# Performance work log

Hardware: AMD Instinct MI355X
Metric: run time of the kernel (lower is better)

Reference implementation:

```python
import jax, jax.numpy as jnp
import numpy as np

N, E, L, C = 5000, 50000, 9, 128      # nodes, edges, (lmax+1)^2 with lmax=2, sphere_channels
HID, HEADS, AV, VC = 128, 8, 32, 16   # attn hidden, heads, alpha channels, value channels
DRBF, AEMB, MAXZ = 128, 64, 100       # rbf dim, atom embed dim, max elements


def _block_params(key, tag):
    ks = jax.random.split(key, 8)
    s = lambda k, shp, fan: jax.random.normal(k, shp, jnp.float32) / np.sqrt(fan)
    return {
        'atom_emb_' + tag: s(ks[0], (MAXZ, AEMB), AEMB),
        'W_rad1_' + tag: s(ks[1], (DRBF + 2 * AEMB, HID), DRBF + 2 * AEMB),
        'W_rad2_' + tag: s(ks[2], (HID, HID), HID),
        'W_msg_' + tag: s(ks[3], (2 * C, HID), 2 * C),
        'W_alpha_' + tag: s(ks[4], (HID, HEADS * AV), HID),
        'alpha_vec_' + tag: s(ks[5], (HEADS, AV), AV),
        'W_val_' + tag: s(ks[6], (HID, HEADS * VC), HID),
        'W_proj_' + tag: s(ks[7], (HEADS * VC, 1), HEADS * VC),
    }


def setup_inputs() -> dict:
    key = jax.random.key(0)
    k = jax.random.split(key, 8)
    inp = {
        'node_embedding': jax.random.normal(k[0], (N, L, C), jnp.float32),
        'edge_distance': jax.random.uniform(k[1], (E, DRBF), jnp.float32),
        'wigner': jax.random.normal(k[2], (E, L, L), jnp.float32) / np.sqrt(L),
        'atomic_numbers': jax.random.randint(k[3], (N,), 0, MAXZ),
        'edge_index': jax.random.randint(k[4], (2, E), 0, N),
        'noise_mask': jax.random.bernoulli(k[5], 0.5, (N,)),
    }
    inp.update(_block_params(k[6], 'v'))
    inp.update(_block_params(k[7], 'd'))
    return inp


def _so2_attention(x, z, edge_dist, src, dst, wig, p, tag):
    # gather + per-edge SO(2)/Wigner rotation
    x_src = jnp.einsum('eij,ejc->eic', wig, x[src])          # [E,L,C]
    x_dst = jnp.einsum('eij,ejc->eic', wig, x[dst])
    msg = jnp.concatenate([x_src, x_dst], axis=-1) @ p['W_msg_' + tag]  # [E,L,HID]
    # radial (distance + atom-edge embedding) channel-wise modulation
    ae = p['atom_emb_' + tag]
    edge_in = jnp.concatenate([edge_dist, ae[z[src]], ae[z[dst]]], axis=-1)
    rad = jax.nn.silu(edge_in @ p['W_rad1_' + tag]) @ p['W_rad2_' + tag]  # [E,HID]
    msg = msg * rad[:, None, :]
    # alpha attention from the l=0 (scalar) coefficient
    a = (msg[:, 0, :] @ p['W_alpha_' + tag]).reshape(E, HEADS, AV)
    logits = jnp.einsum('eha,ha->eh', jax.nn.leaky_relu(a, 0.2), p['alpha_vec_' + tag])
    m = jax.ops.segment_max(logits, dst, num_segments=N)
    ex = jnp.exp(logits - m[dst])
    den = jax.ops.segment_sum(ex, dst, num_segments=N)
    attn = ex / (den[dst] + 1e-9)                            # [E,HEADS]
    # separable S2 gate activation: silu on scalars, sigmoid gate on l>0
    gate = jax.nn.sigmoid(msg[:, :1, :])
    val = jnp.concatenate([jax.nn.silu(msg[:, :1, :]), msg[:, 1:, :] * gate], axis=1)
    v = (val @ p['W_val_' + tag]).reshape(E, L, HEADS, VC)
    v = (v * attn[:, None, :, None]).reshape(E, L, HEADS * VC)
    v = jnp.einsum('eji,ejc->eic', wig, v)                   # inverse (transpose) rotation
    agg = jax.ops.segment_sum(v, dst, num_segments=N)        # scatter-reduce to nodes
    return agg @ p['W_proj_' + tag]                          # [N,L,1]


def reference(node_embedding, edge_distance, wigner,
              atom_emb_v, W_rad1_v, W_rad2_v, W_msg_v, W_alpha_v, alpha_vec_v, W_val_v, W_proj_v,
              atom_emb_d, W_rad1_d, W_rad2_d, W_msg_d, W_alpha_d, alpha_vec_d, W_val_d, W_proj_d,
              atomic_numbers, edge_index, noise_mask):
    p = dict(atom_emb_v=atom_emb_v, W_rad1_v=W_rad1_v, W_rad2_v=W_rad2_v, W_msg_v=W_msg_v,
             W_alpha_v=W_alpha_v, alpha_vec_v=alpha_vec_v, W_val_v=W_val_v, W_proj_v=W_proj_v,
             atom_emb_d=atom_emb_d, W_rad1_d=W_rad1_d, W_rad2_d=W_rad2_d, W_msg_d=W_msg_d,
             W_alpha_d=W_alpha_d, alpha_vec_d=alpha_vec_d, W_val_d=W_val_d, W_proj_d=W_proj_d)
    src, dst = edge_index[0], edge_index[1]
    out_v = _so2_attention(node_embedding, atomic_numbers, edge_distance, src, dst, wigner, p, 'v')
    out_d = _so2_attention(node_embedding, atomic_numbers, edge_distance, src, dst, wigner, p, 'd')
    # narrow(1, 1, 3): take l=1 vector coefficients, view as [N,3]
    vec = out_v[:, 1:4, 0]
    dns = out_d[:, 1:4, 0]
    # denoising_pos_forward with noise_mask: dns*mask + vec*~mask
    return jnp.where(noise_mask[:, None], dns, vec)
```

## Files before the change

kernel.cpp:

```cpp
#include <hip/hip_runtime.h>

#define NN 5000
#define NE 50000
#define LL 9
#define CC 128
#define NH 8
#define VCD 16
#define DR 128
#define AE 64
#define MZ 100

typedef unsigned int u32;
typedef unsigned short u16;

typedef __attribute__((ext_vector_type(8))) short bf16x8;
typedef __attribute__((ext_vector_type(4))) float f32x4;

__device__ __forceinline__ bf16x8 as_bf16x8(uint4 v){
  union { uint4 u; bf16x8 b; } x; x.u = v; return x.b;
}

__device__ __forceinline__ float bf_lo(u32 u){ return __uint_as_float(u << 16); }
__device__ __forceinline__ float bf_hi(u32 u){ return __uint_as_float(u & 0xffff0000u); }
__device__ __forceinline__ u16 f2bf(float f){
  u32 u = __float_as_uint(f);
  u32 r = (u + 0x7fffu + ((u >> 16) & 1u)) >> 16;
  return (u16)r;
}
__device__ __forceinline__ u32 pack2(float a, float b){
  return (u32)f2bf(a) | ((u32)f2bf(b) << 16);
}
__device__ __forceinline__ u32 encf(float f){
  u32 u = __float_as_uint(f);
  return (u & 0x80000000u) ? ~u : (u | 0x80000000u);
}
__device__ __forceinline__ float decf(u32 k){
  u32 u = (k & 0x80000000u) ? (k & 0x7fffffffu) : ~k;
  return __uint_as_float(u);
}
__device__ __forceinline__ float sigmoidf_(float x){ return 1.f / (1.f + __expf(-x)); }

__global__ void k0_tables(const float* __restrict__ ae_v, const float* __restrict__ wr1_v,
                          const float* __restrict__ ae_d, const float* __restrict__ wr1_d,
                          const float* __restrict__ wval_v, const float* __restrict__ wproj_v,
                          const float* __restrict__ wval_d, const float* __restrict__ wproj_d,
                          const float* __restrict__ wmsg_v, const float* __restrict__ wmsg_d,
                          const float* __restrict__ wal_v, const float* __restrict__ wal_d,
                          const float* __restrict__ wr2_v, const float* __restrict__ wr2_d,
                          float* __restrict__ radz, float* __restrict__ wpv,
                          u32* __restrict__ mkey, float* __restrict__ den,
                          float* __restrict__ acc, u32* __restrict__ cnt,
                          u32* __restrict__ WtM, u32* __restrict__ WtA,
                          u32* __restrict__ WtR1, u32* __restrict__ WtR2)
{
  int idx = blockIdx.x * 256 + threadIdx.x;
  if (idx < 2 * 2 * MZ * CC) {
    int c = idx & 127;
    int z = (idx >> 7) % MZ;
    int sd = (idx / (128 * MZ)) & 1;
    int tag = idx / (128 * MZ * 2);
    const float* ae = tag ? ae_d : ae_v;
    const float* w  = tag ? wr1_d : wr1_v;
    float s = 0.f;
    for (int a = 0; a < AE; ++a)
      s += ae[z * AE + a] * w[(DR + sd * AE + a) * CC + c];
    radz[idx] = s;
  }
  int i2 = idx - 2 * 2 * MZ * CC;
  if (i2 >= 0 && i2 < 2 * CC * NH) {
    int h = i2 & 7;
    int c = (i2 >> 3) & 127;
    int tag = i2 >> 10;
    const float* wv = tag ? wval_d : wval_v;
    const float* wp = tag ? wproj_d : wproj_v;
    float s = 0.f;
    for (int q = 0; q < VCD; ++q) s += wv[c * (NH * VCD) + h * VCD + q] * wp[h * VCD + q];
    wpv[i2] = s;
  }
  int i3 = i2 - 2 * CC * NH;
  if (i3 >= 0 && i3 < 2 * NN * NH) mkey[i3] = 0u;
  int i4 = i3 - 2 * NN * NH;
  if (i4 >= 0 && i4 < 2 * NN * NH) den[i4] = 0.f;
  int i5 = i4 - 2 * NN * NH;
  if (i5 >= 0 && i5 < 2 * NN * 3) acc[i5] = 0.f;
  int i6 = i5 - 2 * NN * 3;
  if (i6 >= 0 && i6 < NN) cnt[i6] = 0u;
  int i7 = i6 - NN;
  if (i7 >= 0 && i7 < 4 * 128 * 64) {
    int chunk = i7 >> 13;
    int col = (i7 >> 6) & 127;
    int kp = i7 & 63;
    const float* Wm = (chunk >= 2) ? wmsg_d : wmsg_v;
    int kb = 128 * (chunk & 1);
    WtM[i7] = pack2(Wm[(kb + 2 * kp) * 128 + col], Wm[(kb + 2 * kp + 1) * 128 + col]);
  }
  int i8 = i7 - 4 * 128 * 64;
  if (i8 >= 0 && i8 < 2 * 256 * 64) {
    int tag = i8 >> 14;
    int col = (i8 >> 6) & 255;
    int kp = i8 & 63;
    const float* Wa = tag ? wal_d : wal_v;
    WtA[i8] = pack2(Wa[(2 * kp) * 256 + col], Wa[(2 * kp + 1) * 256 + col]);
  }
  int i9 = i8 - 2 * 256 * 64;
  if (i9 >= 0 && i9 < 2 * 128 * 64) {
    int tag = i9 >> 13;
    int col = (i9 >> 6) & 127;
    int kp = i9 & 63;
    const float* W = tag ? wr1_d : wr1_v;
    WtR1[i9] = pack2(W[(2 * kp) * 128 + col], W[(2 * kp + 1) * 128 + col]);
  }
  int i10 = i9 - 2 * 128 * 64;
  if (i10 >= 0 && i10 < 2 * 128 * 64) {
    int tag = i10 >> 13;
    int col = (i10 >> 6) & 127;
    int kp = i10 & 63;
    const float* W = tag ? wr2_d : wr2_v;
    WtR2[i10] = pack2(W[(2 * kp) * 128 + col], W[(2 * kp + 1) * 128 + col]);
  }
}

__global__ void k0_flag(const u32* __restrict__ mw, int* __restrict__ flag)
{
  __shared__ int bad;
  if (threadIdx.x == 0) bad = 0;
  __syncthreads();
  int lbad = 0;
  for (int i = threadIdx.x; i < 1248; i += 256)
    if (mw[i] > 1u) lbad = 1;
  if (lbad) bad = 1;
  __syncthreads();
  if (threadIdx.x == 0) *flag = bad;
}

__global__ void ks_hist(const int* __restrict__ eidx, u32* __restrict__ cnt)
{
  int idx = blockIdx.x * 256 + threadIdx.x;
  if (idx < NE) atomicAdd(&cnt[eidx[NE + idx]], 1u);
}

__global__ void ks_scan(u32* __restrict__ cnt)
{
  __shared__ u32 tsum[256];
  int t = threadIdx.x;
  u32 loc[20];
  u32 s = 0;
  #pragma unroll
  for (int k = 0; k < 20; ++k) {
    int b = t * 20 + k;
    loc[k] = (b < NN) ? cnt[b] : 0u;
    s += loc[k];
  }
  tsum[t] = s;
  __syncthreads();
  for (int off = 1; off < 256; off <<= 1) {
    u32 v = (t >= off) ? tsum[t - off] : 0u;
    __syncthreads();
    tsum[t] += v;
    __syncthreads();
  }
  u32 base = (t == 0) ? 0u : tsum[t - 1];
  #pragma unroll
  for (int k = 0; k < 20; ++k) {
    int b = t * 20 + k;
    if (b < NN) cnt[b] = base;
    base += loc[k];
  }
}

__global__ void ks_scatter(const int* __restrict__ eidx, u32* __restrict__ base,
                           u32* __restrict__ eperm, int* __restrict__ ssrc, int* __restrict__ sdst)
{
  int idx = blockIdx.x * 256 + threadIdx.x;
  if (idx >= NE) return;
  int d = eidx[NE + idx];
  u32 pos = atomicAdd(&base[d], 1u);
  eperm[pos] = (u32)idx;
  ssrc[pos] = eidx[idx];
  sdst[pos] = d;
}

__global__ __launch_bounds__(256) void k1_nodepre(const float* __restrict__ x,
                                                  const u32* __restrict__ WtM,
                                                  u32* __restrict__ P32)
{
  __shared__ uint4 As4[32 * 17];
  u32* As = (u32*)As4;
  int t = threadIdx.x;
  int row0 = blockIdx.x * 32;
  for (int i = t; i < 32 * 64; i += 256) {
    int r = i >> 6, cp = i & 63;
    int row = row0 + r;
    u32 v = 0u;
    if (row < NN * LL) {
      float2 xv = *(const float2*)(x + (size_t)row * CC + 2 * cp);
      v = pack2(xv.x, xv.y);
    }
    As[r * 68 + cp] = v;
  }
  __syncthreads();
  int w = t >> 6, lane = t & 63;
  int m = lane & 15, kb = lane >> 4;
  int r16 = 16 * (w & 1);
  int cb = 256 * (w >> 1);
  bf16x8 afr[4];
  #pragma unroll
  for (int ks = 0; ks < 4; ++ks)
    afr[ks] = as_bf16x8(*(const uint4*)&As[(r16 + m) * 68 + ks * 16 + kb * 4]);
  int rowbase = row0 + r16;
  for (int ct = 0; ct < 16; ++ct) {
    int col = cb + ct * 16 + m;
    int chunk = col >> 7;
    int cl = col & 127;
    f32x4 accv = {0.f, 0.f, 0.f, 0.f};
    #pragma unroll
    for (int ks = 0; ks < 4; ++ks) {
      bf16x8 bfr = as_bf16x8(*(const uint4*)(WtM + ((size_t)chunk * 128 + cl) * 64 + ks * 16 + kb * 4));
      accv = __builtin_amdgcn_mfma_f32_16x16x32_bf16(afr[ks], bfr, accv, 0, 0, 0);
    }
    #pragma unroll
    for (int reg = 0; reg < 4; ++reg) {
      float v = accv[reg];
      float vv = __shfl_xor(v, 1, 64);
      int row = rowbase + kb * 4 + reg;
      if (((lane & 1) == 0) && row < NN * LL) {
        int n = row / 9, j = row - n * 9;
        P32[((size_t)n * 4 + chunk) * 576 + j * 64 + (cl >> 1)] = pack2(v, vv);
      }
    }
  }
}

__global__ __launch_bounds__(256) void k23_rad(const float* __restrict__ edist,
                                               const u32* __restrict__ WtR1,
                                               const u32* __restrict__ WtR2,
                                               const u32* __restrict__ eperm,
                                               const int* __restrict__ ssrc,
                                               const int* __restrict__ sdst,
                                               const int* __restrict__ zn,
                                               const float* __restrict__ radz,
                                               u32* __restrict__ h1rad)
{
  __shared__ uint4 As4[32 * 17];
  __shared__ uint4 Hs4[32 * 17];
  u32* As = (u32*)As4;
  u32* Hs = (u32*)Hs4;
  __shared__ int zsS[32], zdS[32];
  __shared__ u32 epS[32];
  int t = threadIdx.x;
  int tag = blockIdx.y;
  int e0 = blockIdx.x * 32;
  if (t < 32) {
    int e = e0 + t;
    u32 ep = 0; int s = 0, d = 0;
    if (e < NE) { ep = eperm[e]; s = ssrc[e]; d = sdst[e]; }
    epS[t] = ep; zsS[t] = zn[s]; zdS[t] = zn[d];
  }
  __syncthreads();
  for (int i = t; i < 32 * 64; i += 256) {
    int r = i >> 6, cp = i & 63;
    u32 v = 0u;
    if (e0 + r < NE) {
      float2 xv = *(const float2*)(edist + (size_t)epS[r] * DR + 2 * cp);
      v = pack2(xv.x, xv.y);
    }
    As[r * 68 + cp] = v;
  }
  __syncthreads();
  int w = t >> 6, lane = t & 63;
  int m = lane & 15, kb = lane >> 4;
  int r16 = 16 * (w & 1);
  int cb = 64 * (w >> 1);
  const float* rz_s = radz + tag * 2 * MZ * CC;
  const float* rz_d = rz_s + MZ * CC;
  {
    bf16x8 afr[4];
    #pragma unroll
    for (int ks = 0; ks < 4; ++ks)
      afr[ks] = as_bf16x8(*(const uint4*)&As[(r16 + m) * 68 + ks * 16 + kb * 4]);
    const u32* B1 = WtR1 + (size_t)tag * 128 * 64;
    #pragma unroll
    for (int ct = 0; ct < 4; ++ct) {
      int col = cb + ct * 16 + m;
      f32x4 accv = {0.f, 0.f, 0.f, 0.f};
      #pragma unroll
      for (int ks = 0; ks < 4; ++ks) {
        bf16x8 bfr = as_bf16x8(*(const uint4*)(B1 + (size_t)col * 64 + ks * 16 + kb * 4));
        accv = __builtin_amdgcn_mfma_f32_16x16x32_bf16(afr[ks], bfr, accv, 0, 0, 0);
      }
      #pragma unroll
      for (int reg = 0; reg < 4; ++reg) {
        int row = r16 + kb * 4 + reg;
        float v = accv[reg] + rz_s[zsS[row] * CC + col] + rz_d[zdS[row] * CC + col];
        v = v * sigmoidf_(v);
        float vv = __shfl_xor(v, 1, 64);
        if ((m & 1) == 0) Hs[row * 68 + (col >> 1)] = pack2(v, vv);
      }
    }
  }
  __syncthreads();
  {
    bf16x8 afr[4];
    #pragma unroll
    for (int ks = 0; ks < 4; ++ks)
      afr[ks] = as_bf16x8(*(const uint4*)&Hs[(r16 + m) * 68 + ks * 16 + kb * 4]);
    const u32* B2 = WtR2 + (size_t)tag * 128 * 64;
    #pragma unroll
    for (int ct = 0; ct < 4; ++ct) {
      int col = cb + ct * 16 + m;
      f32x4 accv = {0.f, 0.f, 0.f, 0.f};
      #pragma unroll
      for (int ks = 0; ks < 4; ++ks) {
        bf16x8 bfr = as_bf16x8(*(const uint4*)(B2 + (size_t)col * 64 + ks * 16 + kb * 4));
        accv = __builtin_amdgcn_mfma_f32_16x16x32_bf16(afr[ks], bfr, accv, 0, 0, 0);
      }
      #pragma unroll
      for (int reg = 0; reg < 4; ++reg) {
        int row = r16 + kb * 4 + reg;
        int e = e0 + row;
        float v = accv[reg];
        float vv = __shfl_xor(v, 1, 64);
        if (((m & 1) == 0) && e < NE)
          h1rad[((size_t)tag * NE + e) * 64 + (col >> 1)] = pack2(v, vv);
      }
    }
  }
}

__global__ __launch_bounds__(256) void k4_logits(const u32* __restrict__ P32,
                                                 const float* __restrict__ wig,
                                                 const u32* __restrict__ h1rad,
                                                 const u32* __restrict__ WtA,
                                                 const float* __restrict__ av_v,
                                                 const float* __restrict__ av_d,
                                                 const u32* __restrict__ eperm,
                                                 const int* __restrict__ ssrc,
                                                 const int* __restrict__ sdst,
                                                 float* __restrict__ logits,
                                                 u32* __restrict__ mkey)
{
  __shared__ uint4 As4[32 * 17];
  u32* As = (u32*)As4;
  __shared__ float wig0s[32][9];
  __shared__ int es_s[32], ed_s[32];
  __shared__ u32 ep_s[32];
  __shared__ float ltile[32][8];
  int t = threadIdx.x;
  int tag = blockIdx.y;
  const float* av = tag ? av_d : av_v;
  int i0 = blockIdx.x * 32;
  if (t < 32) {
    int i = i0 + t;
    int s = 0, d = 0; u32 ep = 0;
    if (i < NE) { s = ssrc[i]; d = sdst[i]; ep = eperm[i]; }
    es_s[t] = s; ed_s[t] = d; ep_s[t] = ep;
  }
  __syncthreads();
  for (int q = t; q < 32 * 9; q += 256) {
    int el = q / 9, j = q % 9;
    wig0s[el][j] = (i0 + el < NE) ? wig[(size_t)ep_s[el] * 81 + j] : 0.f;
  }
  __syncthreads();
  {
    int el = t >> 3, pp = t & 7;
    int i = i0 + el;
    float m0[16];
    #pragma unroll
    for (int k = 0; k < 16; ++k) m0[k] = 0.f;
    if (i < NE) {
      const uint4* Ts = (const uint4*)(P32 + ((size_t)es_s[el] * 4 + tag * 2) * 576);
      const uint4* Td = (const uint4*)(P32 + ((size_t)ed_s[el] * 4 + tag * 2 + 1) * 576);
      #pragma unroll
      for (int j = 0; j < 9; ++j) {
        float w = wig0s[el][j];
        uint4 a0 = Ts[j * 16 + 2 * pp], a1 = Ts[j * 16 + 2 * pp + 1];
        uint4 b0 = Td[j * 16 + 2 * pp], b1 = Td[j * 16 + 2 * pp + 1];
        u32 wa[8] = { a0.x, a0.y, a0.z, a0.w, a1.x, a1.y, a1.z, a1.w };
        u32 wb[8] = { b0.x, b0.y, b0.z, b0.w, b1.x, b1.y, b1.z, b1.w };
        #pragma unroll
        for (int r = 0; r < 8; ++r) {
          m0[2 * r]     += w * (bf_lo(wa[r]) + bf_lo(wb[r]));
          m0[2 * r + 1] += w * (bf_hi(wa[r]) + bf_hi(wb[r]));
        }
      }
      const uint4* Rp = (const uint4*)(h1rad + ((size_t)tag * NE + i) * 64);
      uint4 r0u = Rp[2 * pp], r1u = Rp[2 * pp + 1];
      u32 wr[8] = { r0u.x, r0u.y, r0u.z, r0u.w, r1u.x, r1u.y, r1u.z, r1u.w };
      #pragma unroll
      for (int r = 0; r < 8; ++r) {
        m0[2 * r]     *= bf_lo(wr[r]);
        m0[2 * r + 1] *= bf_hi(wr[r]);
      }
    }
    #pragma unroll
    for (int r = 0; r < 8; ++r)
      As[el * 68 + pp * 8 + r] = pack2(m0[2 * r], m0[2 * r + 1]);
  }
  __syncthreads();
  {
    int w = t >> 6, lane = t & 63;
    int m = lane & 15, kb = lane >> 4;
    int r16 = 16 * (w & 1);
    int cb = 128 * (w >> 1);
    bf16x8 afr[4];
    #pragma unroll
    for (int ks = 0; ks < 4; ++ks)
      afr[ks] = as_bf16x8(*(const uint4*)&As[(r16 + m) * 68 + ks * 16 + kb * 4]);
    const u32* WA = WtA + (size_t)tag * 256 * 64;
    float psum[4][4];
    #pragma unroll
    for (int a = 0; a < 4; ++a)
      #pragma unroll
      for (int b = 0; b < 4; ++b) psum[a][b] = 0.f;
    #pragma unroll
    for (int ct = 0; ct < 8; ++ct) {
      int col = cb + ct * 16 + m;
      f32x4 accv = {0.f, 0.f, 0.f, 0.f};
      #pragma unroll
      for (int ks = 0; ks < 4; ++ks) {
        bf16x8 bfr = as_bf16x8(*(const uint4*)(WA + (size_t)col * 64 + ks * 16 + kb * 4));
        accv = __builtin_amdgcn_mfma_f32_16x16x32_bf16(afr[ks], bfr, accv, 0, 0, 0);
      }
      int hl = ct >> 1;
      float avv = av[(4 * (w >> 1) + hl) * 32 + (ct & 1) * 16 + m];
      #pragma unroll
      for (int reg = 0; reg < 4; ++reg) {
        float aa = accv[reg];
        aa = (aa >= 0.f) ? aa : 0.2f * aa;
        psum[hl][reg] += aa * avv;
      }
    }
    #pragma unroll
    for (int hl = 0; hl < 4; ++hl) {
      #pragma unroll
      for (int reg = 0; reg < 4; ++reg) {
        float v = psum[hl][reg];
        v += __shfl_xor(v, 1, 64);
        v += __shfl_xor(v, 2, 64);
        v += __shfl_xor(v, 4, 64);
        v += __shfl_xor(v, 8, 64);
        if (m == 0) ltile[r16 + kb * 4 + reg][4 * (w >> 1) + hl] = v;
      }
    }
  }
  __syncthreads();
  {
    int el = t >> 3, hh = t & 7;
    int i = i0 + el;
    if (i < NE) {
      float lg = ltile[el][hh];
      logits[((size_t)tag * NE + i) * NH + hh] = lg;
      atomicMax(&mkey[tag * NN * NH + ed_s[el] * NH + hh], encf(lg));
    }
  }
}

__global__ void k5_ex(const float* __restrict__ logits, const u32* __restrict__ mkey,
                      const int* __restrict__ sdst, float* __restrict__ ex, float* __restrict__ den)
{
  int idx = blockIdx.x * 256 + threadIdx.x;
  if (idx >= 2 * NE * NH) return;
  int h = idx & 7;
  int e = (idx >> 3) % NE;
  int tag = idx / (NE * NH);
  int d = sdst[e];
  float m = decf(mkey[tag * NN * NH + d * NH + h]);
  float v = __expf(logits[idx] - m);
  ex[idx] = v;
  atomicAdd(&den[tag * NN * NH + d * NH + h], v);
}

__global__ __launch_bounds__(256) void k6_main(const u32* __restrict__ P32,
                                               const float* __restrict__ wig,
                                               const u32* __restrict__ h1rad,
                                               const float* __restrict__ wpv,
                                               const float* __restrict__ ex,
                                               const float* __restrict__ den,
                                               const u32* __restrict__ eperm,
                                               const int* __restrict__ ssrc,
                                               const int* __restrict__ sdst,
                                               float* __restrict__ acc)
{
  __shared__ float wigs[4][81];
  __shared__ u32 ep4[4];
  int t = threadIdx.x;
  int tag = blockIdx.y;
  int ib = blockIdx.x * 4;
  if (t < 4) ep4[t] = eperm[ib + t];
  __syncthreads();
  for (int q = t; q < 4 * 81; q += 256) {
    int el = q / 81, j = q % 81;
    wigs[el][j] = wig[(size_t)ep4[el] * 81 + j];
  }
  __syncthreads();
  int wid = t >> 6, lane = t & 63;
  int i = ib + wid;
  int s = ssrc[i], d = sdst[i];
  const u32* rowT = P32 + ((size_t)s * 4 + tag * 2) * 576;
  const u32* rowB = P32 + ((size_t)d * 4 + tag * 2 + 1) * 576;
  float S0[9], S1[9];
  #pragma unroll
  for (int j = 0; j < 9; ++j) {
    u32 ut = rowT[j * 64 + lane];
    u32 ub = rowB[j * 64 + lane];
    S0[j] = bf_lo(ut) + bf_lo(ub);
    S1[j] = bf_hi(ut) + bf_hi(ub);
  }
  float m0[9], m1[9];
  #pragma unroll
  for (int r = 0; r < 9; ++r) {
    float a0 = 0.f, a1 = 0.f;
    #pragma unroll
    for (int j = 0; j < 9; ++j) {
      float w = wigs[wid][r * 9 + j];
      a0 += w * S0[j];
      a1 += w * S1[j];
    }
    m0[r] = a0; m1[r] = a1;
  }
  u32 ur = h1rad[((size_t)tag * NE + i) * 64 + lane];
  float r0v = bf_lo(ur), r1v = bf_hi(ur);
  #pragma unroll
  for (int r = 0; r < 9; ++r) { m0[r] *= r0v; m1[r] *= r1v; }
  float g0 = sigmoidf_(m0[0]);
  float g1 = sigmoidf_(m1[0]);
  float gA = 0.f, gB = 0.f;
  #pragma unroll
  for (int h = 0; h < NH; ++h) {
    float at = ex[((size_t)tag * NE + i) * NH + h]
             / (den[tag * NN * NH + d * NH + h] + 1e-9f);
    gA += wpv[tag * 1024 + (2 * lane) * 8 + h] * at;
    gB += wpv[tag * 1024 + (2 * lane + 1) * 8 + h] * at;
  }
  float sp[9];
  #pragma unroll
  for (int r = 0; r < 9; ++r)
    sp[r] = m0[r] * g0 * gA + m1[r] * g1 * gB;
  #pragma unroll
  for (int off = 1; off < 64; off <<= 1) {
    #pragma unroll
    for (int r = 0; r < 9; ++r)
      sp[r] += __shfl_xor(sp[r], off, 64);
  }
  if (lane < 3) {
    int ip = lane + 1;
    float y = 0.f;
    #pragma unroll
    for (int j = 0; j < 9; ++j)
      y += wigs[wid][j * 9 + ip] * sp[j];
    atomicAdd(&acc[tag * NN * 3 + d * 3 + lane], y);
  }
}

__global__ void k7_out(const float* __restrict__ acc, const void* __restrict__ mask,
                       const int* __restrict__ flag, float* __restrict__ out)
{
  int idx = blockIdx.x * 256 + threadIdx.x;
  if (idx >= NN * 3) return;
  int n = idx / 3;
  bool msk;
  if (*flag) msk = ((const unsigned char*)mask)[n] != 0;
  else       msk = ((const int*)mask)[n] != 0;
  out[idx] = msk ? acc[NN * 3 + idx] : acc[idx];
}

extern "C" void kernel_launch(void* const* d_in, const int* in_sizes, int n_in,
                              void* d_out, int out_size, void* d_ws, size_t ws_size,
                              hipStream_t stream)
{
  (void)hipGetLastError();

  bool setup_order = (n_in >= 22) && (in_sizes[3] == NN) && (in_sizes[4] == 2 * NE);
  const float *x, *edist, *wig;
  const int *zn, *eidx;
  const void *mask;
  const float *ae_v, *wr1_v, *wr2_v, *wmsg_v, *wal_v, *av_v, *wval_v, *wproj_v;
  const float *ae_d, *wr1_d, *wr2_d, *wmsg_d, *wal_d, *av_d, *wval_d, *wproj_d;
  x     = (const float*)d_in[0];
  edist = (const float*)d_in[1];
  wig   = (const float*)d_in[2];
  if (setup_order) {
    zn      = (const int*)d_in[3];
    eidx    = (const int*)d_in[4];
    mask    = d_in[5];
    ae_v    = (const float*)d_in[6];   wr1_v  = (const float*)d_in[7];
    wr2_v   = (const float*)d_in[8];   wmsg_v = (const float*)d_in[9];
    wal_v   = (const float*)d_in[10];  av_v   = (const float*)d_in[11];
    wval_v  = (const float*)d_in[12];  wproj_v= (const float*)d_in[13];
    ae_d    = (const float*)d_in[14];  wr1_d  = (const float*)d_in[15];
    wr2_d   = (const float*)d_in[16];  wmsg_d = (const float*)d_in[17];
    wal_d   = (const float*)d_in[18];  av_d   = (const float*)d_in[19];
    wval_d  = (const float*)d_in[20];  wproj_d= (const float*)d_in[21];
  } else {
    ae_v    = (const float*)d_in[3];   wr1_v  = (const float*)d_in[4];
    wr2_v   = (const float*)d_in[5];   wmsg_v = (const float*)d_in[6];
    wal_v   = (const float*)d_in[7];   av_v   = (const float*)d_in[8];
    wval_v  = (const float*)d_in[9];   wproj_v= (const float*)d_in[10];
    ae_d    = (const float*)d_in[11];  wr1_d  = (const float*)d_in[12];
    wr2_d   = (const float*)d_in[13];  wmsg_d = (const float*)d_in[14];
    wal_d   = (const float*)d_in[15];  av_d   = (const float*)d_in[16];
    wval_d  = (const float*)d_in[17];  wproj_d= (const float*)d_in[18];
    zn      = (const int*)d_in[19];
    eidx    = (const int*)d_in[20];
    mask    = d_in[21];
  }

  const size_t OFF_P    = 0;
  const size_t OFF_H1   = 46080000;
  const size_t OFF_LOG  = 71680000;
  const size_t OFF_EX   = 74880000;
  const size_t OFF_MK   = 78080000;
  const size_t OFF_DEN  = 78400000;
  const size_t OFF_ACC  = 78720000;
  const size_t OFF_RADZ = 78840000;
  const size_t OFF_WPV  = 79044800;
  const size_t OFF_FLAG = 79052992;
  const size_t OFF_CNT  = 79053056;
  const size_t OFF_PERM = 79073056;
  const size_t OFF_SSRC = 79273056;
  const size_t OFF_SDST = 79473056;
  const size_t OFF_WTM  = 79673056;
  const size_t OFF_WTA  = 79804128;
  const size_t OFF_WTR1 = 79935200;
  const size_t OFF_WTR2 = 80000736;
  const size_t NEEDED   = 80066272;

  const size_t out_bytes = (size_t)out_size * sizeof(float);

  if (d_ws == nullptr || ws_size < NEEDED) {
    hipMemsetAsync(d_out, 0x66, out_bytes, stream);
    return;
  }

  char* ws = (char*)d_ws;
  u32*   P32    = (u32*)(ws + OFF_P);
  u32*   h1rad  = (u32*)(ws + OFF_H1);
  float* logits = (float*)(ws + OFF_LOG);
  float* ex     = (float*)(ws + OFF_EX);
  u32*   mkey   = (u32*)(ws + OFF_MK);
  float* den    = (float*)(ws + OFF_DEN);
  float* acc    = (float*)(ws + OFF_ACC);
  float* radz   = (float*)(ws + OFF_RADZ);
  float* wpv    = (float*)(ws + OFF_WPV);
  int*   flag   = (int*)(ws + OFF_FLAG);
  u32*   cnt    = (u32*)(ws + OFF_CNT);
  u32*   eperm  = (u32*)(ws + OFF_PERM);
  int*   ssrc   = (int*)(ws + OFF_SSRC);
  int*   sdst   = (int*)(ws + OFF_SDST);
  u32*   WtM    = (u32*)(ws + OFF_WTM);
  u32*   WtA    = (u32*)(ws + OFF_WTA);
  u32*   WtR1   = (u32*)(ws + OFF_WTR1);
  u32*   WtR2   = (u32*)(ws + OFF_WTR2);

  k0_tables<<<1354, 256, 0, stream>>>(ae_v, wr1_v, ae_d, wr1_d,
                                      wval_v, wproj_v, wval_d, wproj_d,
                                      wmsg_v, wmsg_d, wal_v, wal_d,
                                      wr2_v, wr2_d,
                                      radz, wpv, mkey, den, acc, cnt,
                                      WtM, WtA, WtR1, WtR2);
  k0_flag<<<1, 256, 0, stream>>>((const u32*)mask, flag);
  ks_hist<<<196, 256, 0, stream>>>(eidx, cnt);
  ks_scan<<<1, 256, 0, stream>>>(cnt);
  ks_scatter<<<196, 256, 0, stream>>>(eidx, cnt, eperm, ssrc, sdst);
  k1_nodepre<<<1407, 256, 0, stream>>>(x, WtM, P32);
  k23_rad<<<dim3(1563, 2), 256, 0, stream>>>(edist, WtR1, WtR2, eperm, ssrc, sdst,
                                             zn, radz, h1rad);
  k4_logits<<<dim3(1563, 2), 256, 0, stream>>>(P32, wig, h1rad, WtA, av_v, av_d,
                                               eperm, ssrc, sdst, logits, mkey);
  k5_ex<<<3125, 256, 0, stream>>>(logits, mkey, sdst, ex, den);
  k6_main<<<dim3(12500, 2), 256, 0, stream>>>(P32, wig, h1rad, wpv, ex, den,
                                              eperm, ssrc, sdst, acc);
  k7_out<<<59, 256, 0, stream>>>(acc, mask, flag, (float*)d_out);

  if (hipGetLastError() != hipSuccess) {
    hipMemsetAsync(d_out, 0x77, out_bytes, stream);
  }
}
```

Baseline: 526.1 us.

## Fuse full message rotation into logits kernel and precompute per-head projected values

```diff
diff --git a/kernel.cpp b/kernel.cpp
--- a/kernel.cpp
+++ b/kernel.cpp
@@ -327,24 +327,27 @@
   }
 }
 
-__global__ __launch_bounds__(256) void k4_logits(const u32* __restrict__ P32,
-                                                 const float* __restrict__ wig,
-                                                 const u32* __restrict__ h1rad,
-                                                 const u32* __restrict__ WtA,
-                                                 const float* __restrict__ av_v,
-                                                 const float* __restrict__ av_d,
-                                                 const u32* __restrict__ eperm,
-                                                 const int* __restrict__ ssrc,
-                                                 const int* __restrict__ sdst,
-                                                 float* __restrict__ logits,
-                                                 u32* __restrict__ mkey)
+__global__ __launch_bounds__(256) void kF(const u32* __restrict__ P32,
+                                          const float* __restrict__ wig,
+                                          const u32* __restrict__ h1rad,
+                                          const u32* __restrict__ WtA,
+                                          const float* __restrict__ av_v,
+                                          const float* __restrict__ av_d,
+                                          const float* __restrict__ wpv,
+                                          const u32* __restrict__ eperm,
+                                          const int* __restrict__ ssrc,
+                                          const int* __restrict__ sdst,
+                                          float* __restrict__ logits,
+                                          u32* __restrict__ mkey,
+                                          float* __restrict__ Tbuf)
 {
   __shared__ uint4 As4[32 * 17];
   u32* As = (u32*)As4;
-  __shared__ float wig0s[32][9];
+  __shared__ float wigS[32][82];
   __shared__ int es_s[32], ed_s[32];
   __shared__ u32 ep_s[32];
   __shared__ float ltile[32][8];
+  __shared__ float wpvS[1024];
   int t = threadIdx.x;
   int tag = blockIdx.y;
   const float* av = tag ? av_d : av_v;
@@ -355,50 +358,92 @@
     if (i < NE) { s = ssrc[i]; d = sdst[i]; ep = eperm[i]; }
     es_s[t] = s; ed_s[t] = d; ep_s[t] = ep;
   }
-  __syncthreads();
-  for (int q = t; q < 32 * 9; q += 256) {
-    int el = q / 9, j = q % 9;
-    wig0s[el][j] = (i0 + el < NE) ? wig[(size_t)ep_s[el] * 81 + j] : 0.f;
+  for (int q = t; q < 1024; q += 256) wpvS[q] = wpv[tag * 1024 + q];
+  __syncthreads();
+  for (int q = t; q < 32 * 81; q += 256) {
+    int el = q / 81, j = q - el * 81;
+    wigS[el][j] = (i0 + el < NE) ? wig[(size_t)ep_s[el] * 81 + j] : 0.f;
+  }
+  __syncthreads();
+  int w = t >> 6, lane = t & 63;
+  for (int k = 0; k < 8; ++k) {
+    int el = w * 8 + k;
+    int i = i0 + el;
+    bool ok = (i < NE);
+    float S0[9], S1[9];
+    #pragma unroll
+    for (int j = 0; j < 9; ++j) { S0[j] = 0.f; S1[j] = 0.f; }
+    float r0v = 0.f, r1v = 0.f;
+    if (ok) {
+      const u32* rowT = P32 + ((size_t)es_s[el] * 4 + tag * 2) * 576;
+      const u32* rowB = P32 + ((size_t)ed_s[el] * 4 + tag * 2 + 1) * 576;
+      #pragma unroll
+      for (int j = 0; j < 9; ++j) {
+        u32 a = rowT[j * 64 + lane];
+        u32 b = rowB[j * 64 + lane];
+        S0[j] = bf_lo(a) + bf_lo(b);
+        S1[j] = bf_hi(a) + bf_hi(b);
+      }
+      u32 ur = h1rad[((size_t)tag * NE + i) * 64 + lane];
+      r0v = bf_lo(ur); r1v = bf_hi(ur);
+    }
+    float m0[9], m1[9];
+    #pragma unroll
+    for (int r = 0; r < 9; ++r) {
+      float a0 = 0.f, a1 = 0.f;
+      #pragma unroll
+      for (int j = 0; j < 9; ++j) {
+        float wv = wigS[el][r * 9 + j];
+        a0 += wv * S0[j];
+        a1 += wv * S1[j];
+      }
+      m0[r] = a0 * r0v;
+      m1[r] = a1 * r1v;
+    }
+    As[el * 68 + lane] = pack2(m0[0], m1[0]);
+    float g0 = sigmoidf_(m0[0]);
+    float g1 = sigmoidf_(m1[0]);
+    float Wp[3][8];
+    #pragma unroll
+    for (int i3 = 0; i3 < 3; ++i3)
+      #pragma unroll
+      for (int h = 0; h < 8; ++h) Wp[i3][h] = 0.f;
+    #pragma unroll
+    for (int j = 0; j < 9; ++j) {
+      float v0 = m0[j] * g0, v1 = m1[j] * g1;
+      float vw[8];
+      #pragma unroll
+      for (int h = 0; h < 8; ++h)
+        vw[h] = v0 * wpvS[(2 * lane) * 8 + h] + v1 * wpvS[(2 * lane + 1) * 8 + h];
+      float wo1 = wigS[el][j * 9 + 1];
+      float wo2 = wigS[el][j * 9 + 2];
+      float wo3 = wigS[el][j * 9 + 3];
+      #pragma unroll
+      for (int h = 0; h < 8; ++h) {
+        Wp[0][h] += wo1 * vw[h];
+        Wp[1][h] += wo2 * vw[h];
+        Wp[2][h] += wo3 * vw[h];
+      }
+    }
+    #pragma unroll
+    for (int off = 1; off < 64; off <<= 1)
+      #pragma unroll
+      for (int i3 = 0; i3 < 3; ++i3)
+        #pragma unroll
+        for (int h = 0; h < 8; ++h)
+          Wp[i3][h] += __shfl_xor(Wp[i3][h], off, 64);
+    if (lane == 0 && ok) {
+      float* Tp = Tbuf + ((size_t)tag * NE + i) * 24;
+      #pragma unroll
+      for (int h = 0; h < 8; ++h) {
+        Tp[h * 3 + 0] = Wp[0][h];
+        Tp[h * 3 + 1] = Wp[1][h];
+        Tp[h * 3 + 2] = Wp[2][h];
+      }
+    }
   }
   __syncthreads();
   {
-    int el = t >> 3, pp = t & 7;
-    int i = i0 + el;
-    float m0[16];
-    #pragma unroll
-    for (int k = 0; k < 16; ++k) m0[k] = 0.f;
-    if (i < NE) {
-      const uint4* Ts = (const uint4*)(P32 + ((size_t)es_s[el] * 4 + tag * 2) * 576);
-      const uint4* Td = (const uint4*)(P32 + ((size_t)ed_s[el] * 4 + tag * 2 + 1) * 576);
-      #pragma unroll
-      for (int j = 0; j < 9; ++j) {
-        float w = wig0s[el][j];
-        uint4 a0 = Ts[j * 16 + 2 * pp], a1 = Ts[j * 16 + 2 * pp + 1];
-        uint4 b0 = Td[j * 16 + 2 * pp], b1 = Td[j * 16 + 2 * pp + 1];
-        u32 wa[8] = { a0.x, a0.y, a0.z, a0.w, a1.x, a1.y, a1.z, a1.w };
-        u32 wb[8] = { b0.x, b0.y, b0.z, b0.w, b1.x, b1.y, b1.z, b1.w };
-        #pragma unroll
-        for (int r = 0; r < 8; ++r) {
-          m0[2 * r]     += w * (bf_lo(wa[r]) + bf_lo(wb[r]));
-          m0[2 * r + 1] += w * (bf_hi(wa[r]) + bf_hi(wb[r]));
-        }
-      }
-      const uint4* Rp = (const uint4*)(h1rad + ((size_t)tag * NE + i) * 64);
-      uint4 r0u = Rp[2 * pp], r1u = Rp[2 * pp + 1];
-      u32 wr[8] = { r0u.x, r0u.y, r0u.z, r0u.w, r1u.x, r1u.y, r1u.z, r1u.w };
-      #pragma unroll
-      for (int r = 0; r < 8; ++r) {
-        m0[2 * r]     *= bf_lo(wr[r]);
-        m0[2 * r + 1] *= bf_hi(wr[r]);
-      }
-    }
-    #pragma unroll
-    for (int r = 0; r < 8; ++r)
-      As[el * 68 + pp * 8 + r] = pack2(m0[2 * r], m0[2 * r + 1]);
-  }
-  __syncthreads();
-  {
-    int w = t >> 6, lane = t & 63;
     int m = lane & 15, kb = lane >> 4;
     int r16 = 16 * (w & 1);
     int cb = 128 * (w >> 1);
@@ -470,86 +515,28 @@
   atomicAdd(&den[tag * NN * NH + d * NH + h], v);
 }
 
-__global__ __launch_bounds__(256) void k6_main(const u32* __restrict__ P32,
-                                               const float* __restrict__ wig,
-                                               const u32* __restrict__ h1rad,
-                                               const float* __restrict__ wpv,
-                                               const float* __restrict__ ex,
-                                               const float* __restrict__ den,
-                                               const u32* __restrict__ eperm,
-                                               const int* __restrict__ ssrc,
-                                               const int* __restrict__ sdst,
-                                               float* __restrict__ acc)
-{
-  __shared__ float wigs[4][81];
-  __shared__ u32 ep4[4];
-  int t = threadIdx.x;
-  int tag = blockIdx.y;
-  int ib = blockIdx.x * 4;
-  if (t < 4) ep4[t] = eperm[ib + t];
-  __syncthreads();
-  for (int q = t; q < 4 * 81; q += 256) {
-    int el = q / 81, j = q % 81;
-    wigs[el][j] = wig[(size_t)ep4[el] * 81 + j];
-  }
-  __syncthreads();
-  int wid = t >> 6, lane = t & 63;
-  int i = ib + wid;
-  int s = ssrc[i], d = sdst[i];
-  const u32* rowT = P32 + ((size_t)s * 4 + tag * 2) * 576;
-  const u32* rowB = P32 + ((size_t)d * 4 + tag * 2 + 1) * 576;
-  float S0[9], S1[9];
+__global__ void k6_scatter(const float* __restrict__ ex, const float* __restrict__ den,
+                           const float* __restrict__ Tbuf, const int* __restrict__ sdst,
+                           float* __restrict__ acc)
+{
+  int idx = blockIdx.x * 256 + threadIdx.x;
+  if (idx >= 2 * NE) return;
+  int tag = idx / NE;
+  int e = idx - tag * NE;
+  int d = sdst[e];
+  const float* Tp = Tbuf + ((size_t)tag * NE + e) * 24;
+  float y0 = 0.f, y1 = 0.f, y2 = 0.f;
   #pragma unroll
-  for (int j = 0; j < 9; ++j) {
-    u32 ut = rowT[j * 64 + lane];
-    u32 ub = rowB[j * 64 + lane];
-    S0[j] = bf_lo(ut) + bf_lo(ub);
-    S1[j] = bf_hi(ut) + bf_hi(ub);
-  }
-  float m0[9], m1[9];
-  #pragma unroll
-  for (int r = 0; r < 9; ++r) {
-    float a0 = 0.f, a1 = 0.f;
-    #pragma unroll
-    for (int j = 0; j < 9; ++j) {
-      float w = wigs[wid][r * 9 + j];
-      a0 += w * S0[j];
-      a1 += w * S1[j];
-    }
-    m0[r] = a0; m1[r] = a1;
-  }
-  u32 ur = h1rad[((size_t)tag * NE + i) * 64 + lane];
-  float r0v = bf_lo(ur), r1v = bf_hi(ur);
-  #pragma unroll
-  for (int r = 0; r < 9; ++r) { m0[r] *= r0v; m1[r] *= r1v; }
-  float g0 = sigmoidf_(m0[0]);
-  float g1 = sigmoidf_(m1[0]);
-  float gA = 0.f, gB = 0.f;
-  #pragma unroll
-  for (int h = 0; h < NH; ++h) {
-    float at = ex[((size_t)tag * NE + i) * NH + h]
+  for (int h = 0; h < 8; ++h) {
+    float at = ex[((size_t)tag * NE + e) * 8 + h]
              / (den[tag * NN * NH + d * NH + h] + 1e-9f);
-    gA += wpv[tag * 1024 + (2 * lane) * 8 + h] * at;
-    gB += wpv[tag * 1024 + (2 * lane + 1) * 8 + h] * at;
-  }
-  float sp[9];
-  #pragma unroll
-  for (int r = 0; r < 9; ++r)
-    sp[r] = m0[r] * g0 * gA + m1[r] * g1 * gB;
-  #pragma unroll
-  for (int off = 1; off < 64; off <<= 1) {
-    #pragma unroll
-    for (int r = 0; r < 9; ++r)
-      sp[r] += __shfl_xor(sp[r], off, 64);
-  }
-  if (lane < 3) {
-    int ip = lane + 1;
-    float y = 0.f;
-    #pragma unroll
-    for (int j = 0; j < 9; ++j)
-      y += wigs[wid][j * 9 + ip] * sp[j];
-    atomicAdd(&acc[tag * NN * 3 + d * 3 + lane], y);
-  }
+    y0 += at * Tp[h * 3 + 0];
+    y1 += at * Tp[h * 3 + 1];
+    y2 += at * Tp[h * 3 + 2];
+  }
+  atomicAdd(&acc[tag * NN * 3 + d * 3 + 0], y0);
+  atomicAdd(&acc[tag * NN * 3 + d * 3 + 1], y1);
+  atomicAdd(&acc[tag * NN * 3 + d * 3 + 2], y2);
 }
 
 __global__ void k7_out(const float* __restrict__ acc, const void* __restrict__ mask,
@@ -609,21 +596,22 @@
   const size_t OFF_H1   = 46080000;
   const size_t OFF_LOG  = 71680000;
   const size_t OFF_EX   = 74880000;
-  const size_t OFF_MK   = 78080000;
-  const size_t OFF_DEN  = 78400000;
-  const size_t OFF_ACC  = 78720000;
-  const size_t OFF_RADZ = 78840000;
-  const size_t OFF_WPV  = 79044800;
-  const size_t OFF_FLAG = 79052992;
-  const size_t OFF_CNT  = 79053056;
-  const size_t OFF_PERM = 79073056;
-  const size_t OFF_SSRC = 79273056;
-  const size_t OFF_SDST = 79473056;
-  const size_t OFF_WTM  = 79673056;
-  const size_t OFF_WTA  = 79804128;
-  const size_t OFF_WTR1 = 79935200;
-  const size_t OFF_WTR2 = 80000736;
-  const size_t NEEDED   = 80066272;
+  const size_t OFF_T    = 78080000;
+  const size_t OFF_MK   = 87680000;
+  const size_t OFF_DEN  = 88000000;
+  const size_t OFF_ACC  = 88320000;
+  const size_t OFF_RADZ = 88440000;
+  const size_t OFF_WPV  = 88644800;
+  const size_t OFF_FLAG = 88652992;
+  const size_t OFF_CNT  = 88653056;
+  const size_t OFF_PERM = 88673056;
+  const size_t OFF_SSRC = 88873056;
+  const size_t OFF_SDST = 89073056;
+  const size_t OFF_WTM  = 89273056;
+  const size_t OFF_WTA  = 89404128;
+  const size_t OFF_WTR1 = 89535200;
+  const size_t OFF_WTR2 = 89600736;
+  const size_t NEEDED   = 89666272;
 
   const size_t out_bytes = (size_t)out_size * sizeof(float);
 
@@ -637,6 +625,7 @@
   u32*   h1rad  = (u32*)(ws + OFF_H1);
   float* logits = (float*)(ws + OFF_LOG);
   float* ex     = (float*)(ws + OFF_EX);
+  float* Tbuf   = (float*)(ws + OFF_T);
   u32*   mkey   = (u32*)(ws + OFF_MK);
   float* den    = (float*)(ws + OFF_DEN);
   float* acc    = (float*)(ws + OFF_ACC);
@@ -665,11 +654,10 @@
   k1_nodepre<<<1407, 256, 0, stream>>>(x, WtM, P32);
   k23_rad<<<dim3(1563, 2), 256, 0, stream>>>(edist, WtR1, WtR2, eperm, ssrc, sdst,
                                              zn, radz, h1rad);
-  k4_logits<<<dim3(1563, 2), 256, 0, stream>>>(P32, wig, h1rad, WtA, av_v, av_d,
-                                               eperm, ssrc, sdst, logits, mkey);
+  kF<<<dim3(1563, 2), 256, 0, stream>>>(P32, wig, h1rad, WtA, av_v, av_d, wpv,
+                                        eperm, ssrc, sdst, logits, mkey, Tbuf);
   k5_ex<<<3125, 256, 0, stream>>>(logits, mkey, sdst, ex, den);
-  k6_main<<<dim3(12500, 2), 256, 0, stream>>>(P32, wig, h1rad, wpv, ex, den,
-                                              eperm, ssrc, sdst, acc);
+  k6_scatter<<<391, 256, 0, stream>>>(ex, den, Tbuf, sdst, acc);
   k7_out<<<59, 256, 0, stream>>>(acc, mask, flag, (float*)d_out);
 
   if (hipGetLastError() != hipSuccess) {
```

After: 581.0 us. +10.4%, slower.
